# Performance work log

Measured on AMD Instinct MI355X. Metric: run time of the kernel, lower is better.

## Reference

```python
import jax, jax.numpy as jnp
import numpy as np
from jax import lax

EPS = 1e-5

def _groupnorm1(v, scale, bias):
    # GroupNorm(1, C) on [bs, C] vectors (spatial dims are 1x1): normalize over C per sample
    m = jnp.mean(v, axis=-1, keepdims=True)
    var = jnp.mean((v - m) ** 2, axis=-1, keepdims=True)
    return (v - m) / jnp.sqrt(var + EPS) * scale + bias

def _mish(v):
    return v * jnp.tanh(jax.nn.softplus(v))


def setup_inputs() -> dict:
    key = jax.random.key(0)
    ks = jax.random.split(key, 5)
    bs, C, H, W = 32, 128, 64, 64
    K, red = 4, 16
    hid = C // red
    return {
        "x": jax.random.normal(ks[0], (bs, C, H, W), jnp.float32),
        "weight": jax.random.normal(ks[1], (K, C, C, 3, 3), jnp.float32) * 0.05,
        "bias": jax.random.normal(ks[2], (K, C), jnp.float32) * 0.05,
        "se_w1": jax.random.normal(ks[3], (hid, C), jnp.float32) * 0.1,
        "gn1_scale": jnp.ones((hid,), jnp.float32),
        "gn1_bias": jnp.zeros((hid,), jnp.float32),
        "se_w2": jax.random.normal(ks[4], (K, hid), jnp.float32) * 0.1,
        "gn2_scale": jnp.ones((K,), jnp.float32),
        "gn2_bias": jnp.zeros((K,), jnp.float32),
    }


def reference(x, weight, bias, se_w1, gn1_scale, gn1_bias, se_w2, gn2_scale, gn2_bias):
    bs, C, H, W = x.shape
    K, out_p, in_p, kh, kw = weight.shape

    # --- SqueezeAndExcitation attention -> [bs, K] in (0,1) ---
    pooled = jnp.mean(x, axis=(2, 3))                       # [bs, C]
    h1 = pooled @ se_w1.T                                   # [bs, hid] (1x1 conv, no bias)
    h1 = _mish(_groupnorm1(h1, gn1_scale, gn1_bias))
    h2 = h1 @ se_w2.T                                       # [bs, K]
    att = jax.nn.sigmoid(_groupnorm1(h2, gn2_scale, gn2_bias))

    # --- per-sample kernel / bias aggregation ---
    agg_w = jnp.einsum('bk,koihw->boihw', att, weight)      # [bs, out, in, kh, kw]
    agg_b = att @ bias                                      # [bs, out]

    # --- per-sample conv2d (equivalent to groups=bs grouped conv in torch) ---
    pad = ((1, 1), (1, 1))
    def per_sample(xi, wi):
        return lax.conv_general_dilated(
            xi[None], wi, window_strides=(1, 1), padding=pad,
            dimension_numbers=('NCHW', 'OIHW', 'NCHW'))[0]
    out = jax.vmap(per_sample)(x, agg_w)                    # [bs, out, H, W]
    return out + agg_b[:, :, None, None]
```

## Files before the change

kernel.cpp:

```cpp
#include <hip/hip_runtime.h>
#include <hip/hip_bf16.h>
#include <math.h>
#include <stdint.h>

#define EPS 1e-5f

typedef __attribute__((ext_vector_type(8))) short bf16x8;
typedef __attribute__((ext_vector_type(16))) float f32x16;

__device__ __forceinline__ ushort f2bf(float f) {
    union { float f; unsigned u; } v; v.f = f;
    unsigned r = (v.u + 0x7FFFu + ((v.u >> 16) & 1u)) >> 16;
    return (ushort)r;
}

__device__ __forceinline__ void dma16(const void* g, void* l) {
    __builtin_amdgcn_global_load_lds(
        (__attribute__((address_space(1))) const void*)(uintptr_t)g,
        (__attribute__((address_space(3))) void*)(uintptr_t)l,
        16, 0, 0);
}

__global__ __launch_bounds__(256) void transpose_kernel(const float* __restrict__ x,
                                                        ushort* __restrict__ xT,
                                                        float* __restrict__ partial) {
    __shared__ float T2[64][132];
    int bid = blockIdx.x;
    int b = (bid & 7) * 4 + (bid >> 9);
    int y = (bid >> 3) & 63;
    int t = threadIdx.x;

    int ic2 = t >> 1, half = t & 1;
    const float4* src = (const float4*)(x + (((size_t)b * 128 + ic2) * 64 + y) * 64 + half * 32);
    float s = 0.f;
#pragma unroll
    for (int i = 0; i < 8; ++i) {
        float4 v = src[i];
        int c0 = half * 32 + i * 4;
        T2[c0][ic2] = v.x; T2[c0 + 1][ic2] = v.y; T2[c0 + 2][ic2] = v.z; T2[c0 + 3][ic2] = v.w;
        s += v.x + v.y + v.z + v.w;
    }
    s += __shfl_xor(s, 1, 64);
    if (half == 0) partial[((size_t)b * 64 + y) * 128 + ic2] = s;
    __syncthreads();

    int col = t >> 2, icq = t & 3;
    const float4* row = (const float4*)&T2[col][icq * 32];
    uint pk[16];
#pragma unroll
    for (int m = 0; m < 8; ++m) {
        float4 v = row[m];
        pk[2 * m]     = (uint)f2bf(v.x) | ((uint)f2bf(v.y) << 16);
        pk[2 * m + 1] = (uint)f2bf(v.z) | ((uint)f2bf(v.w) << 16);
    }
    ushort* dst = xT + (((size_t)(b * 66 + y + 1)) * 66 + col + 1) * 128 + icq * 32;
    ((uint4*)dst)[0] = make_uint4(pk[0], pk[1], pk[2], pk[3]);
    ((uint4*)dst)[1] = make_uint4(pk[4], pk[5], pk[6], pk[7]);
    ((uint4*)dst)[2] = make_uint4(pk[8], pk[9], pk[10], pk[11]);
    ((uint4*)dst)[3] = make_uint4(pk[12], pk[13], pk[14], pk[15]);

    uint4 z = make_uint4(0, 0, 0, 0);
    if (y == 0) {
        uint4* row0 = (uint4*)(xT + ((size_t)b * 66 + 0) * 66 * 128);
        for (int i = t; i < 1056; i += 256) row0[i] = z;
    }
    if (y == 63) {
        uint4* row65 = (uint4*)(xT + ((size_t)b * 66 + 65) * 66 * 128);
        for (int i = t; i < 1056; i += 256) row65[i] = z;
    }
    if (t < 32) {
        int c = (t >> 4) * 65;
        int i = t & 15;
        *(uint4*)(xT + (((size_t)(b * 66 + y + 1)) * 66 + c) * 128 + i * 8) = z;
    }
}

__global__ __launch_bounds__(256) void sefuse_kernel(const float* __restrict__ partial,
                                                     const float* __restrict__ se_w1,
                                                     const float* __restrict__ gn1_s, const float* __restrict__ gn1_b,
                                                     const float* __restrict__ se_w2,
                                                     const float* __restrict__ gn2_s, const float* __restrict__ gn2_b,
                                                     float* __restrict__ att) {
    __shared__ float sA[256];
    __shared__ float pl[128];
    __shared__ float h1s[8];
    int b = blockIdx.x;
    int t = threadIdx.x;
    int ic = t & 127, hf = t >> 7;

    const float* p = partial + ((size_t)b * 64 + hf * 32) * 128 + ic;
    float s = 0.f;
#pragma unroll
    for (int k = 0; k < 32; ++k) s += p[k * 128];
    sA[t] = s;
    __syncthreads();
    if (t < 128) pl[t] = (sA[t] + sA[t + 128]) * (1.0f / 4096.0f);
    __syncthreads();
    if (t < 8) {
        float s1 = 0.f;
        for (int c = 0; c < 128; ++c) s1 += pl[c] * se_w1[t * 128 + c];
        h1s[t] = s1;
    }
    __syncthreads();
    if (t == 0) {
        float h1[8];
#pragma unroll
        for (int j = 0; j < 8; ++j) h1[j] = h1s[j];
        float m = 0.f;
#pragma unroll
        for (int j = 0; j < 8; ++j) m += h1[j];
        m *= 0.125f;
        float var = 0.f;
#pragma unroll
        for (int j = 0; j < 8; ++j) { float d = h1[j] - m; var += d * d; }
        var *= 0.125f;
        float inv = rsqrtf(var + EPS);
#pragma unroll
        for (int j = 0; j < 8; ++j) {
            float tt = (h1[j] - m) * inv * gn1_s[j] + gn1_b[j];
            float sp = (tt > 20.f) ? tt : log1pf(expf(tt));
            h1[j] = tt * tanhf(sp);
        }
        float h2[4];
#pragma unroll
        for (int k = 0; k < 4; ++k) {
            float s2 = 0.f;
#pragma unroll
            for (int j = 0; j < 8; ++j) s2 += h1[j] * se_w2[k * 8 + j];
            h2[k] = s2;
        }
        float m2 = 0.25f * (h2[0] + h2[1] + h2[2] + h2[3]);
        float v2 = 0.f;
#pragma unroll
        for (int k = 0; k < 4; ++k) { float d = h2[k] - m2; v2 += d * d; }
        v2 *= 0.25f;
        float inv2 = rsqrtf(v2 + EPS);
#pragma unroll
        for (int k = 0; k < 4; ++k) {
            float tt = (h2[k] - m2) * inv2 * gn2_s[k] + gn2_b[k];
            att[b * 4 + k] = 1.0f / (1.0f + expf(-tt));
        }
    }
}

__global__ __launch_bounds__(256) void aggw_kernel(const float* __restrict__ weight,
                                                   const float* __restrict__ att,
                                                   ushort* __restrict__ aggw) {
    int tq = (blockIdx.x % 72) * 256 + threadIdx.x;
    int rep = blockIdx.x / 72;
    int tap = tq >> 10;
    int within = tq & 1023;
    int oc = within >> 3;
    int p = within & 7;
    int g = (p - oc) & 7;
    int h = tap / 9, s = tap % 9;
    int ic0 = h * 64 + g * 8;

    float wv[4][8];
#pragma unroll
    for (int k = 0; k < 4; ++k)
#pragma unroll
        for (int j = 0; j < 8; ++j)
            wv[k][j] = weight[(((size_t)(k * 128 + oc)) * 128 + ic0 + j) * 9 + s];

    for (int b = rep * 8; b < rep * 8 + 8; ++b) {
        float a0 = att[b * 4 + 0], a1 = att[b * 4 + 1], a2 = att[b * 4 + 2], a3 = att[b * 4 + 3];
        uint pk[4];
#pragma unroll
        for (int q = 0; q < 4; ++q) {
            float f0 = a0 * wv[0][2 * q] + a1 * wv[1][2 * q] + a2 * wv[2][2 * q] + a3 * wv[3][2 * q];
            float f1 = a0 * wv[0][2 * q + 1] + a1 * wv[1][2 * q + 1] + a2 * wv[2][2 * q + 1] + a3 * wv[3][2 * q + 1];
            pk[q] = (uint)f2bf(f0) | ((uint)f2bf(f1) << 16);
        }
        *(uint4*)(aggw + (size_t)b * 147456 + (size_t)tq * 8) = make_uint4(pk[0], pk[1], pk[2], pk[3]);
    }
}

__global__ __launch_bounds__(256, 2) void conv_kernel(const ushort* __restrict__ xT,
                                                      const ushort* __restrict__ aggw,
                                                      const float* __restrict__ att,
                                                      const float* __restrict__ bias,
                                                      float* __restrict__ out) {
    __shared__ ushort ldsB[2][12672];

    int bid = blockIdx.x;
    int xcd = bid & 7;
    int idx = bid >> 3;
    int b = xcd * 4 + (idx >> 4);
    int tile = idx & 15;
    int y0 = tile * 4;

    int tid = threadIdx.x;
    int l = tid & 63, w = tid >> 6;
    int wm = w >> 1, wn = w & 1;
    int l31 = l & 31, lhi = l >> 5;

    const ushort* xTb = xT + ((size_t)(b * 66 + y0)) * 66 * 128;
    const ushort* Asmp = aggw + (size_t)b * 147456;

    int ocofs[2], rotA[2];
#pragma unroll
    for (int mi = 0; mi < 2; ++mi) {
        int oc = wm * 64 + mi * 32 + l31;
        ocofs[mi] = oc * 64;
        rotA[mi] = (lhi + oc) & 7;
    }

    f32x16 acc[2][4];
#pragma unroll
    for (int mi = 0; mi < 2; ++mi)
#pragma unroll
        for (int nb = 0; nb < 4; ++nb)
#pragma unroll
            for (int q = 0; q < 16; ++q) acc[mi][nb][q] = 0.f;

    bf16x8 aR[3][2][2];

#define LOADA(R, Q, S)                                                                       \
    {                                                                                        \
        const ushort* tb_ = Asmp + (size_t)((((Q) >> 1) * 9 + (S))) * 8192;                  \
        _Pragma("unroll")                                                                    \
        for (int ib_ = 0; ib_ < 2; ++ib_)                                                    \
            _Pragma("unroll")                                                                \
            for (int mi_ = 0; mi_ < 2; ++mi_)                                                \
                aR[R][ib_][mi_] = *(const bf16x8*)(tb_ + ocofs[mi_] +                        \
                    (((rotA[mi_] + 4 * ((Q) & 1) + 2 * ib_) & 7) << 3));                     \
    }

#define STAGE(Q, BUF)                                                                        \
    {                                                                                        \
        _Pragma("unroll")                                                                    \
        for (int i_ = 0; i_ < 7; ++i_) {                                                     \
            int k_ = i_ * 256 + tid;                                                         \
            if (k_ < 1584) {                                                                 \
                int rc_ = k_ >> 2;                                                           \
                int p_ = k_ & 3;                                                             \
                int c_ = rc_ % 66;                                                           \
                int g_ = (p_ - c_ - (c_ >> 2)) & 3;                                          \
                dma16(xTb + (size_t)rc_ * 128 + (Q) * 32 + (g_ << 3),                        \
                      &ldsB[BUF][(size_t)k_ * 8]);                                           \
            }                                                                                \
        }                                                                                    \
    }

    STAGE(0, 0);
    LOADA(0, 0, 0);
    LOADA(1, 0, 1);
    __syncthreads();

    for (int q = 0; q < 4; ++q) {
        int cur = q & 1;
        if (q < 3) {
            if (cur) { STAGE(q + 1, 0); } else { STAGE(q + 1, 1); }
        }
        const ushort* buf = ldsB[cur];
#pragma unroll
        for (int s = 0; s < 9; ++s) {
            const int kh = s / 3, kw = s - kh * 3;
            {
                bf16x8 bb[4];
#pragma unroll
                for (int nb = 0; nb < 4; ++nb) {
                    int r = 2 * wn + (nb >> 1) + kh;
                    int c = (nb & 1) * 32 + l31 + kw;
                    int p = (lhi + c + (c >> 2)) & 3;
                    bb[nb] = *(const bf16x8*)&buf[((r * 66 + c) << 5) + (p << 3)];
                }
                __builtin_amdgcn_s_setprio(1);
#pragma unroll
                for (int mi = 0; mi < 2; ++mi)
#pragma unroll
                    for (int nb = 0; nb < 4; ++nb)
                        acc[mi][nb] = __builtin_amdgcn_mfma_f32_32x32x16_bf16(aR[s % 3][0][mi], bb[nb], acc[mi][nb], 0, 0, 0);
                __builtin_amdgcn_s_setprio(0);
            }
            if (q < 3 || s < 7) {
                if (s < 7) { LOADA((s + 2) % 3, q, s + 2); }
                else if (s == 7) { LOADA(0, q + 1, 0); }
                else { LOADA(1, q + 1, 1); }
            }
            {
                bf16x8 bb[4];
#pragma unroll
                for (int nb = 0; nb < 4; ++nb) {
                    int r = 2 * wn + (nb >> 1) + kh;
                    int c = (nb & 1) * 32 + l31 + kw;
                    int p = (2 + lhi + c + (c >> 2)) & 3;
                    bb[nb] = *(const bf16x8*)&buf[((r * 66 + c) << 5) + (p << 3)];
                }
                __builtin_amdgcn_s_setprio(1);
#pragma unroll
                for (int mi = 0; mi < 2; ++mi)
#pragma unroll
                    for (int nb = 0; nb < 4; ++nb)
                        acc[mi][nb] = __builtin_amdgcn_mfma_f32_32x32x16_bf16(aR[s % 3][1][mi], bb[nb], acc[mi][nb], 0, 0, 0);
                __builtin_amdgcn_s_setprio(0);
            }
        }
        __syncthreads();
    }

    float a0 = att[b * 4 + 0], a1 = att[b * 4 + 1], a2 = att[b * 4 + 2], a3 = att[b * 4 + 3];
#pragma unroll
    for (int mi = 0; mi < 2; ++mi)
#pragma unroll
        for (int q = 0; q < 16; ++q) {
            int oc = wm * 64 + mi * 32 + (q & 3) + 8 * (q >> 2) + 4 * lhi;
            float ab = a0 * bias[oc] + a1 * bias[128 + oc] + a2 * bias[256 + oc] + a3 * bias[384 + oc];
#pragma unroll
            for (int nb = 0; nb < 4; ++nb) {
                int y = y0 + 2 * wn + (nb >> 1);
                out[(((size_t)b * 128 + oc) * 64 + y) * 64 + (nb & 1) * 32 + l31] = acc[mi][nb][q] + ab;
            }
        }
#undef LOADA
#undef STAGE
}

extern "C" void kernel_launch(void* const* d_in, const int* in_sizes, int n_in,
                              void* d_out, int out_size, void* d_ws, size_t ws_size,
                              hipStream_t stream) {
    const float* x      = (const float*)d_in[0];
    const float* weight = (const float*)d_in[1];
    const float* bias   = (const float*)d_in[2];
    const float* se_w1  = (const float*)d_in[3];
    const float* gn1_s  = (const float*)d_in[4];
    const float* gn1_b  = (const float*)d_in[5];
    const float* se_w2  = (const float*)d_in[6];
    const float* gn2_s  = (const float*)d_in[7];
    const float* gn2_b  = (const float*)d_in[8];
    float* out = (float*)d_out;

    float*  att     = (float*)((char*)d_ws + 16384);
    float*  partial = (float*)((char*)d_ws + 65536);
    ushort* aggw    = (ushort*)((char*)d_ws + 65536);
    ushort* xT      = (ushort*)((char*)d_ws + 10485760);

    transpose_kernel<<<2048, 256, 0, stream>>>(x, xT, partial);
    sefuse_kernel<<<32, 256, 0, stream>>>(partial, se_w1, gn1_s, gn1_b, se_w2, gn2_s, gn2_b, att);
    aggw_kernel<<<288, 256, 0, stream>>>(weight, att, aggw);
    conv_kernel<<<512, 256, 0, stream>>>(xT, aggw, att, bias, out);
}
```

Before: 102.4 us.

## Fuse SE into aggw, use atomic pooling, quarter-split input layout, bigger conv tiles

Pooling now uses atomics into a zeroed buffer. The SE attention is computed redundantly inside each aggregation block, which drops the separate sefuse kernel. The transposed input is stored as four channel-quarter planes so each conv stage loads contiguous slabs. The conv kernel goes to 512 threads with 8-row tiles, uses finer vmcnt waits instead of full syncthreads, and drops setprio. In exchange it adds a memset launch, adds atomic contention, and gives the conv kernel half the blocks and a larger LDS footprint.

After: 104.9 us. +2.4%, slower.

```diff
diff --git a/kernel.cpp b/kernel.cpp
--- a/kernel.cpp
+++ b/kernel.cpp
@@ -22,9 +22,9 @@
 }
 
 __global__ __launch_bounds__(256) void transpose_kernel(const float* __restrict__ x,
-                                                        ushort* __restrict__ xT,
-                                                        float* __restrict__ partial) {
-    __shared__ float T2[64][132];
+                                                        ushort* __restrict__ xTq,
+                                                        float* __restrict__ pooled) {
+    __shared__ float T[128][68];
     int bid = blockIdx.x;
     int b = (bid & 7) * 4 + (bid >> 9);
     int y = (bid >> 3) & 63;
@@ -32,80 +32,79 @@
 
     int ic2 = t >> 1, half = t & 1;
     const float4* src = (const float4*)(x + (((size_t)b * 128 + ic2) * 64 + y) * 64 + half * 32);
+    float4* trow = (float4*)&T[ic2][half * 32];
     float s = 0.f;
 #pragma unroll
     for (int i = 0; i < 8; ++i) {
         float4 v = src[i];
-        int c0 = half * 32 + i * 4;
-        T2[c0][ic2] = v.x; T2[c0 + 1][ic2] = v.y; T2[c0 + 2][ic2] = v.z; T2[c0 + 3][ic2] = v.w;
+        trow[i] = v;
         s += v.x + v.y + v.z + v.w;
     }
     s += __shfl_xor(s, 1, 64);
-    if (half == 0) partial[((size_t)b * 64 + y) * 128 + ic2] = s;
+    if (half == 0) atomicAdd(&pooled[b * 128 + ic2], s * (1.0f / 4096.0f));
     __syncthreads();
 
-    int col = t >> 2, icq = t & 3;
-    const float4* row = (const float4*)&T2[col][icq * 32];
+    int col = t & 63, icq = t >> 6;
     uint pk[16];
 #pragma unroll
-    for (int m = 0; m < 8; ++m) {
-        float4 v = row[m];
-        pk[2 * m]     = (uint)f2bf(v.x) | ((uint)f2bf(v.y) << 16);
-        pk[2 * m + 1] = (uint)f2bf(v.z) | ((uint)f2bf(v.w) << 16);
-    }
-    ushort* dst = xT + (((size_t)(b * 66 + y + 1)) * 66 + col + 1) * 128 + icq * 32;
+    for (int jj = 0; jj < 16; ++jj) {
+        float f0 = T[icq * 32 + 2 * jj][col];
+        float f1 = T[icq * 32 + 2 * jj + 1][col];
+        pk[jj] = (uint)f2bf(f0) | ((uint)f2bf(f1) << 16);
+    }
+    ushort* dst = xTq + ((((size_t)(b * 4 + icq) * 66) + y + 1) * 66 + col + 1) * 32;
     ((uint4*)dst)[0] = make_uint4(pk[0], pk[1], pk[2], pk[3]);
     ((uint4*)dst)[1] = make_uint4(pk[4], pk[5], pk[6], pk[7]);
     ((uint4*)dst)[2] = make_uint4(pk[8], pk[9], pk[10], pk[11]);
     ((uint4*)dst)[3] = make_uint4(pk[12], pk[13], pk[14], pk[15]);
 
     uint4 z = make_uint4(0, 0, 0, 0);
-    if (y == 0) {
-        uint4* row0 = (uint4*)(xT + ((size_t)b * 66 + 0) * 66 * 128);
-        for (int i = t; i < 1056; i += 256) row0[i] = z;
-    }
-    if (y == 63) {
-        uint4* row65 = (uint4*)(xT + ((size_t)b * 66 + 65) * 66 * 128);
-        for (int i = t; i < 1056; i += 256) row65[i] = z;
+    if (y == 0 || y == 63) {
+        int row = (y == 0) ? 0 : 65;
+        for (int i = t; i < 1056; i += 256) {
+            int qq = i / 264, rr = i - qq * 264;
+            *(((uint4*)(xTq + (((size_t)(b * 4 + qq) * 66 + row) * 66) * 32)) + rr) = z;
+        }
     }
     if (t < 32) {
-        int c = (t >> 4) * 65;
-        int i = t & 15;
-        *(uint4*)(xT + (((size_t)(b * 66 + y + 1)) * 66 + c) * 128 + i * 8) = z;
-    }
-}
-
-__global__ __launch_bounds__(256) void sefuse_kernel(const float* __restrict__ partial,
-                                                     const float* __restrict__ se_w1,
-                                                     const float* __restrict__ gn1_s, const float* __restrict__ gn1_b,
-                                                     const float* __restrict__ se_w2,
-                                                     const float* __restrict__ gn2_s, const float* __restrict__ gn2_b,
-                                                     float* __restrict__ att) {
-    __shared__ float sA[256];
-    __shared__ float pl[128];
-    __shared__ float h1s[8];
-    int b = blockIdx.x;
+        int qq = t >> 3, cc = ((t >> 2) & 1) * 65, part = t & 3;
+        *(uint4*)(xTq + ((((size_t)(b * 4 + qq) * 66) + y + 1) * 66 + cc) * 32 + part * 8) = z;
+    }
+}
+
+__global__ __launch_bounds__(256) void aggw_kernel(const float* __restrict__ weight,
+                                                   const float* __restrict__ pooled,
+                                                   const float* __restrict__ se_w1,
+                                                   const float* __restrict__ gn1_s, const float* __restrict__ gn1_b,
+                                                   const float* __restrict__ se_w2,
+                                                   const float* __restrict__ gn2_s, const float* __restrict__ gn2_b,
+                                                   float* __restrict__ att_out,
+                                                   ushort* __restrict__ aggw) {
+    __shared__ float pl[8][128];
+    __shared__ float h1s[8][8];
+    __shared__ float att_s[8][4];
+    int blk = blockIdx.x;
+    int rep = blk / 72;
     int t = threadIdx.x;
-    int ic = t & 127, hf = t >> 7;
-
-    const float* p = partial + ((size_t)b * 64 + hf * 32) * 128 + ic;
-    float s = 0.f;
-#pragma unroll
-    for (int k = 0; k < 32; ++k) s += p[k * 128];
-    sA[t] = s;
+
+#pragma unroll
+    for (int u = 0; u < 4; ++u) {
+        int pid = u * 256 + t;
+        int bl = pid >> 7, ic = pid & 127;
+        pl[bl][ic] = pooled[(rep * 8 + bl) * 128 + ic];
+    }
     __syncthreads();
-    if (t < 128) pl[t] = (sA[t] + sA[t + 128]) * (1.0f / 4096.0f);
+    if (t < 64) {
+        int bl = t >> 3, jj = t & 7;
+        float s1 = 0.f;
+        for (int c = 0; c < 128; ++c) s1 += pl[bl][c] * se_w1[jj * 128 + c];
+        h1s[bl][jj] = s1;
+    }
     __syncthreads();
     if (t < 8) {
-        float s1 = 0.f;
-        for (int c = 0; c < 128; ++c) s1 += pl[c] * se_w1[t * 128 + c];
-        h1s[t] = s1;
-    }
-    __syncthreads();
-    if (t == 0) {
         float h1[8];
 #pragma unroll
-        for (int j = 0; j < 8; ++j) h1[j] = h1s[j];
+        for (int j = 0; j < 8; ++j) h1[j] = h1s[t][j];
         float m = 0.f;
 #pragma unroll
         for (int j = 0; j < 8; ++j) m += h1[j];
@@ -138,16 +137,14 @@
 #pragma unroll
         for (int k = 0; k < 4; ++k) {
             float tt = (h2[k] - m2) * inv2 * gn2_s[k] + gn2_b[k];
-            att[b * 4 + k] = 1.0f / (1.0f + expf(-tt));
-        }
-    }
-}
-
-__global__ __launch_bounds__(256) void aggw_kernel(const float* __restrict__ weight,
-                                                   const float* __restrict__ att,
-                                                   ushort* __restrict__ aggw) {
-    int tq = (blockIdx.x % 72) * 256 + threadIdx.x;
-    int rep = blockIdx.x / 72;
+            att_s[t][k] = 1.0f / (1.0f + expf(-tt));
+        }
+    }
+    __syncthreads();
+
+    if ((blk % 72) == 0 && t < 32) att_out[rep * 32 + t] = att_s[t >> 2][t & 3];
+
+    int tq = (blk % 72) * 256 + t;
     int tap = tq >> 10;
     int within = tq & 1023;
     int oc = within >> 3;
@@ -163,8 +160,10 @@
         for (int j = 0; j < 8; ++j)
             wv[k][j] = weight[(((size_t)(k * 128 + oc)) * 128 + ic0 + j) * 9 + s];
 
-    for (int b = rep * 8; b < rep * 8 + 8; ++b) {
-        float a0 = att[b * 4 + 0], a1 = att[b * 4 + 1], a2 = att[b * 4 + 2], a3 = att[b * 4 + 3];
+#pragma unroll
+    for (int bl = 0; bl < 8; ++bl) {
+        int b = rep * 8 + bl;
+        float a0 = att_s[bl][0], a1 = att_s[bl][1], a2 = att_s[bl][2], a3 = att_s[bl][3];
         uint pk[4];
 #pragma unroll
         for (int q = 0; q < 4; ++q) {
@@ -176,26 +175,25 @@
     }
 }
 
-__global__ __launch_bounds__(256, 2) void conv_kernel(const ushort* __restrict__ xT,
+__global__ __launch_bounds__(512, 2) void conv_kernel(const ushort* __restrict__ xTq,
                                                       const ushort* __restrict__ aggw,
                                                       const float* __restrict__ att,
                                                       const float* __restrict__ bias,
                                                       float* __restrict__ out) {
-    __shared__ ushort ldsB[2][12672];
+    __shared__ ushort ldsQ[2][21120];
 
     int bid = blockIdx.x;
     int xcd = bid & 7;
     int idx = bid >> 3;
-    int b = xcd * 4 + (idx >> 4);
-    int tile = idx & 15;
-    int y0 = tile * 4;
+    int b = xcd * 4 + (idx >> 3);
+    int tile = idx & 7;
+    int y0 = tile * 8;
 
     int tid = threadIdx.x;
     int l = tid & 63, w = tid >> 6;
-    int wm = w >> 1, wn = w & 1;
+    int wm = w >> 2, wn = w & 3;
     int l31 = l & 31, lhi = l >> 5;
 
-    const ushort* xTb = xT + ((size_t)(b * 66 + y0)) * 66 * 128;
     const ushort* Asmp = aggw + (size_t)b * 147456;
 
     int ocofs[2], rotA[2];
@@ -229,31 +227,35 @@
 
 #define STAGE(Q, BUF)                                                                        \
     {                                                                                        \
+        const ushort* qb_ = xTq + (((size_t)(b * 4 + (Q)) * 66 + y0)) * 66 * 32;             \
         _Pragma("unroll")                                                                    \
-        for (int i_ = 0; i_ < 7; ++i_) {                                                     \
-            int k_ = i_ * 256 + tid;                                                         \
-            if (k_ < 1584) {                                                                 \
+        for (int i_ = 0; i_ < 6; ++i_) {                                                     \
+            int k_ = i_ * 512 + tid;                                                         \
+            if (k_ < 2640) {                                                                 \
                 int rc_ = k_ >> 2;                                                           \
                 int p_ = k_ & 3;                                                             \
-                int c_ = rc_ % 66;                                                           \
+                int r_ = rc_ / 66;                                                           \
+                int c_ = rc_ - r_ * 66;                                                      \
                 int g_ = (p_ - c_ - (c_ >> 2)) & 3;                                          \
-                dma16(xTb + (size_t)rc_ * 128 + (Q) * 32 + (g_ << 3),                        \
-                      &ldsB[BUF][(size_t)k_ * 8]);                                           \
+                dma16(qb_ + ((size_t)rc_) * 32 + (g_ << 3), &ldsQ[BUF][(size_t)k_ * 8]);     \
             }                                                                                \
         }                                                                                    \
     }
 
     STAGE(0, 0);
+    __builtin_amdgcn_sched_barrier(0);
     LOADA(0, 0, 0);
     LOADA(1, 0, 1);
-    __syncthreads();
+    asm volatile("s_waitcnt vmcnt(8)" ::: "memory");
+    __builtin_amdgcn_s_barrier();
+    __builtin_amdgcn_sched_barrier(0);
 
     for (int q = 0; q < 4; ++q) {
-        int cur = q & 1;
+        const ushort* buf = ldsQ[q & 1];
         if (q < 3) {
-            if (cur) { STAGE(q + 1, 0); } else { STAGE(q + 1, 1); }
-        }
-        const ushort* buf = ldsB[cur];
+            if ((q & 1) == 0) { STAGE(q + 1, 1); } else { STAGE(q + 1, 0); }
+            __builtin_amdgcn_sched_barrier(0);
+        }
 #pragma unroll
         for (int s = 0; s < 9; ++s) {
             const int kh = s / 3, kw = s - kh * 3;
@@ -261,18 +263,16 @@
                 bf16x8 bb[4];
 #pragma unroll
                 for (int nb = 0; nb < 4; ++nb) {
-                    int r = 2 * wn + (nb >> 1) + kh;
                     int c = (nb & 1) * 32 + l31 + kw;
+                    int cell = (2 * wn + (nb >> 1) + kh) * 66 + c;
                     int p = (lhi + c + (c >> 2)) & 3;
-                    bb[nb] = *(const bf16x8*)&buf[((r * 66 + c) << 5) + (p << 3)];
+                    bb[nb] = *(const bf16x8*)&buf[(cell << 5) + (p << 3)];
                 }
-                __builtin_amdgcn_s_setprio(1);
 #pragma unroll
                 for (int mi = 0; mi < 2; ++mi)
 #pragma unroll
                     for (int nb = 0; nb < 4; ++nb)
                         acc[mi][nb] = __builtin_amdgcn_mfma_f32_32x32x16_bf16(aR[s % 3][0][mi], bb[nb], acc[mi][nb], 0, 0, 0);
-                __builtin_amdgcn_s_setprio(0);
             }
             if (q < 3 || s < 7) {
                 if (s < 7) { LOADA((s + 2) % 3, q, s + 2); }
@@ -283,21 +283,23 @@
                 bf16x8 bb[4];
 #pragma unroll
                 for (int nb = 0; nb < 4; ++nb) {
-                    int r = 2 * wn + (nb >> 1) + kh;
                     int c = (nb & 1) * 32 + l31 + kw;
+                    int cell = (2 * wn + (nb >> 1) + kh) * 66 + c;
                     int p = (2 + lhi + c + (c >> 2)) & 3;
-                    bb[nb] = *(const bf16x8*)&buf[((r * 66 + c) << 5) + (p << 3)];
+                    bb[nb] = *(const bf16x8*)&buf[(cell << 5) + (p << 3)];
                 }
-                __builtin_amdgcn_s_setprio(1);
 #pragma unroll
                 for (int mi = 0; mi < 2; ++mi)
 #pragma unroll
                     for (int nb = 0; nb < 4; ++nb)
                         acc[mi][nb] = __builtin_amdgcn_mfma_f32_32x32x16_bf16(aR[s % 3][1][mi], bb[nb], acc[mi][nb], 0, 0, 0);
-                __builtin_amdgcn_s_setprio(0);
             }
         }
-        __syncthreads();
+        if (q < 3) {
+            asm volatile("s_waitcnt vmcnt(36)" ::: "memory");
+            __builtin_amdgcn_s_barrier();
+            __builtin_amdgcn_sched_barrier(0);
+        }
     }
 
     float a0 = att[b * 4 + 0], a1 = att[b * 4 + 1], a2 = att[b * 4 + 2], a3 = att[b * 4 + 3];
@@ -331,13 +333,14 @@
     const float* gn2_b  = (const float*)d_in[8];
     float* out = (float*)d_out;
 
-    float*  att     = (float*)((char*)d_ws + 16384);
-    float*  partial = (float*)((char*)d_ws + 65536);
-    ushort* aggw    = (ushort*)((char*)d_ws + 65536);
-    ushort* xT      = (ushort*)((char*)d_ws + 10485760);
-
-    transpose_kernel<<<2048, 256, 0, stream>>>(x, xT, partial);
-    sefuse_kernel<<<32, 256, 0, stream>>>(partial, se_w1, gn1_s, gn1_b, se_w2, gn2_s, gn2_b, att);
-    aggw_kernel<<<288, 256, 0, stream>>>(weight, att, aggw);
-    conv_kernel<<<512, 256, 0, stream>>>(xT, aggw, att, bias, out);
-}
+    float*  att    = (float*)d_ws;
+    float*  pooled = (float*)((char*)d_ws + 16384);
+    ushort* aggw   = (ushort*)((char*)d_ws + 65536);
+    ushort* xTq    = (ushort*)((char*)d_ws + 10485760);
+
+    hipMemsetAsync(pooled, 0, 128 * 32 * sizeof(float), stream);
+    transpose_kernel<<<2048, 256, 0, stream>>>(x, xTq, pooled);
+    aggw_kernel<<<288, 256, 0, stream>>>(weight, pooled, se_w1, gn1_s, gn1_b,
+                                         se_w2, gn2_s, gn2_b, att, aggw);
+    conv_kernel<<<256, 512, 0, stream>>>(xTq, aggw, att, bias, out);
+}
```
